# Kernel tuning notes

Measured on AMD Instinct MI355X. Metric: run time of the kernel, lower is better.

The kernel has to match this reference:

```python
import jax, jax.numpy as jnp
import numpy as np

K = 20
EPS = 1e-5
NEG_SLOPE = 0.2


def knn_idx(feat, k):
    # feat: (B, N, C). Pairwise neg squared distance, top-k nearest (self included).
    inner = jnp.einsum('bnc,bmc->bnm', feat, feat)          # (B,N,N)
    sq = jnp.sum(feat * feat, axis=-1)                      # (B,N)
    pd = 2.0 * inner - sq[:, :, None] - sq[:, None, :]      # -||xi-xj||^2
    return jax.lax.top_k(pd, k)[1]                          # (B,N,k)


def edge_conv(feat, W, g, b, m, v, k):
    # feat: (B,N,C); W: (O, 2C); BN params over O channels (eval-mode BN).
    idx = knn_idx(feat, k)                                  # (B,N,k)
    nbr = jnp.take_along_axis(feat[:, None, :, :], idx[..., None], axis=2)  # (B,N,k,C)
    ctr = jnp.broadcast_to(feat[:, :, None, :], nbr.shape)
    edge = jnp.concatenate([nbr - ctr, ctr], axis=-1)       # (B,N,k,2C)
    h = jnp.einsum('bnkc,oc->bnko', edge, W)                # 1x1 conv
    h = (h - m) * (g / jnp.sqrt(v + EPS)) + b               # BatchNorm2d (eval)
    h = jnp.where(h >= 0, h, NEG_SLOPE * h)                 # LeakyReLU(0.2)
    return jnp.max(h, axis=2)                               # max over k -> (B,N,O)


def setup_inputs() -> dict:
    key = jax.random.key(0)
    ks = jax.random.split(key, 21)
    B, N, C = 4, 4096, 3
    d = {'x': jax.random.normal(ks[0], (B, N, C), dtype=jnp.float32)}
    dims = [(64, 2 * 3), (64, 2 * 64), (128, 2 * 64), (256, 2 * 128)]
    for i, (o, c) in enumerate(dims, start=1):
        j = 1 + (i - 1) * 5
        d[f'W{i}'] = jax.random.normal(ks[j], (o, c), dtype=jnp.float32) * (1.0 / np.sqrt(c))
        d[f'g{i}'] = jax.random.uniform(ks[j + 1], (o,), minval=0.5, maxval=1.5, dtype=jnp.float32)
        d[f'b{i}'] = jax.random.normal(ks[j + 2], (o,), dtype=jnp.float32) * 0.1
        d[f'm{i}'] = jax.random.normal(ks[j + 3], (o,), dtype=jnp.float32) * 0.1
        d[f'v{i}'] = jax.random.uniform(ks[j + 4], (o,), minval=0.5, maxval=1.5, dtype=jnp.float32)
    return d


def reference(x, W1, g1, b1, m1, v1, W2, g2, b2, m2, v2,
              W3, g3, b3, m3, v3, W4, g4, b4, m4, v4):
    x1 = edge_conv(x, W1, g1, b1, m1, v1, K)    # (B,N,64)
    x2 = edge_conv(x1, W2, g2, b2, m2, v2, K)   # (B,N,64)
    x3 = edge_conv(x2, W3, g3, b3, m3, v3, K)   # (B,N,128)
    x4 = edge_conv(x3, W4, g4, b4, m4, v4, K)   # (B,N,256)
    return x4
```

## Files before the change

kernel.cpp:

```cpp
#include <hip/hip_runtime.h>

#define NTOT 4096
#define NBATCH 4
#define KNN 20
#define JSPLIT 8
#define JSPLIT3 4
#define KMRG 28
#define CSLOT3 256
#define CSLOTM 512

constexpr float NEG_INF = -3.0e38f;

typedef __attribute__((ext_vector_type(8))) short bf16x8;
typedef __attribute__((ext_vector_type(4))) float f32x4;

__device__ __forceinline__ unsigned pk(float f, int j) {
  unsigned u = __float_as_uint(f);
  u = (u & 0x80000000u) ? ~u : (u | 0x80000000u);
  return (u & 0xFFFFF000u) | (unsigned)j;
}

__device__ __forceinline__ void pins16(unsigned u, unsigned (&tv)[16]) {
  if (u > tv[0]) {
    tv[0] = u;
#pragma unroll
    for (int x = 1; x < 16; x++) {
      unsigned mn = min(tv[0], tv[x]);
      unsigned mx = max(tv[0], tv[x]);
      tv[0] = mn;
      tv[x] = mx;
    }
  }
}

__device__ __forceinline__ void pins8(unsigned u, unsigned (&tv)[8]) {
  if (u > tv[0]) {
    tv[0] = u;
#pragma unroll
    for (int x = 1; x < 8; x++) {
      unsigned mn = min(tv[0], tv[x]);
      unsigned mx = max(tv[0], tv[x]);
      tv[0] = mn;
      tv[x] = mx;
    }
  }
}

__device__ __forceinline__ void gll16(const void* g, void* l) {
  __builtin_amdgcn_global_load_lds(
      (const __attribute__((address_space(1))) unsigned int*)g,
      (__attribute__((address_space(3))) unsigned int*)l, 16, 0, 0);
}

__global__ void prep_w(const float* __restrict__ W, const float* __restrict__ gg,
                       const float* __restrict__ bb, const float* __restrict__ mm,
                       const float* __restrict__ vv, float* __restrict__ Wc,
                       float* __restrict__ bias, int O, int C) {
  int t = blockIdx.x * 256 + threadIdx.x;
  if (t >= 2 * O * C) return;
  int o2 = t / C, c = t - o2 * C;
  int o = (o2 < O) ? o2 : o2 - O;
  float s = gg[o] * rsqrtf(vv[o] + 1e-5f);
  float w = (o2 < O) ? W[o * 2 * C + c] * s
                     : (W[o * 2 * C + C + c] - W[o * 2 * C + c]) * s;
  Wc[o2 * C + c] = w;
  if (o2 >= O && c == 0) bias[o] = bb[o] - mm[o] * s;
}

__global__ void cvt_k(const float* __restrict__ f, ushort* __restrict__ hi,
                      ushort* __restrict__ lo) {
  int p = blockIdx.x * 256 + threadIdx.x;
  float x = f[p];
  unsigned u = __float_as_uint(x);
  unsigned h = (u + 0x7FFFu + ((u >> 16) & 1u)) >> 16;
  float hf = __uint_as_float(h << 16);
  float r = x - hf;
  unsigned v = __float_as_uint(r);
  unsigned l = (v + 0x7FFFu + ((v >> 16) & 1u)) >> 16;
  hi[p] = (ushort)h;
  lo[p] = (ushort)l;
}

template <int C>
__global__ void sqh_k(const float* __restrict__ f, float* __restrict__ sqh) {
  int p = blockIdx.x * 256 + threadIdx.x;
  const float* r = f + (size_t)p * C;
  float s = 0.f;
#pragma unroll
  for (int c4 = 0; c4 < C / 4; c4++) {
    float4 v = *(const float4*)&r[c4 * 4];
    s += v.x * v.x + v.y * v.y + v.z * v.z + v.w * v.w;
  }
  sqh[p] = 0.5f * s;
}

__global__ __launch_bounds__(256) void knn3_g(const float* __restrict__ feat,
                                              unsigned* __restrict__ cval) {
  __shared__ __align__(16) float sA[64 * 4];

  int tid = threadIdx.x;
  int js = blockIdx.x & (JSPLIT3 - 1);
  int rb = (blockIdx.x >> 2) & 63;
  int b = blockIdx.x >> 8;
  int row0 = rb * 64;
  int r = tid >> 2, q = tid & 3;
  int i = row0 + r;
  const float* fb = feat + (size_t)b * NTOT * 3;

  float c0 = fb[(size_t)i * 3 + 0];
  float c1 = fb[(size_t)i * 3 + 1];
  float c2 = fb[(size_t)i * 3 + 2];

  unsigned tv[16];
#pragma unroll
  for (int t = 0; t < 16; t++) tv[t] = 0u;

  for (int jt = js * (NTOT / JSPLIT3); jt < (js + 1) * (NTOT / JSPLIT3); jt += 64) {
    __syncthreads();
    if (tid < 64) {
      sA[tid * 4 + 0] = fb[(size_t)(jt + tid) * 3 + 0];
      sA[tid * 4 + 1] = fb[(size_t)(jt + tid) * 3 + 1];
      sA[tid * 4 + 2] = fb[(size_t)(jt + tid) * 3 + 2];
    }
    __syncthreads();

#pragma unroll
    for (int cc = 0; cc < 4; cc++) {
      float vq[4];
#pragma unroll
      for (int u = 0; u < 4; u++) {
        int jl = (cc * 4 + u) * 4 + q;
        float d0 = c0 - sA[jl * 4];
        float d1 = c1 - sA[jl * 4 + 1];
        float d2 = c2 - sA[jl * 4 + 2];
        vq[u] = -(d0 * d0 + d1 * d1 + d2 * d2);
      }
      float m4 = fmaxf(fmaxf(vq[0], vq[1]), fmaxf(vq[2], vq[3]));
      if (pk(m4, 0xFFF) > tv[0]) {
#pragma unroll
        for (int u = 0; u < 4; u++)
          pins16(pk(vq[u], jt + (cc * 4 + u) * 4 + q), tv);
      }
    }
  }

  int p = b * NTOT + row0 + r;
  int sub = js * 4 + q;
  unsigned* dst = cval + (size_t)p * CSLOT3 + sub * 16;
#pragma unroll
  for (int t4 = 0; t4 < 4; t4++) {
    uint4 o;
    o.x = tv[t4 * 4 + 0];
    o.y = tv[t4 * 4 + 1];
    o.z = tv[t4 * 4 + 2];
    o.w = tv[t4 * 4 + 3];
    *(uint4*)&dst[t4 * 4] = o;
  }
}

template <int C>
__global__ __launch_bounds__(256, 2) void knn_m(const ushort* __restrict__ Xhi,
                                                const ushort* __restrict__ Xlo,
                                                const float* __restrict__ sqh,
                                                unsigned* __restrict__ cval) {
  constexpr int NK = C / 32;
  constexpr int NJT = NTOT / (128 * JSPLIT);
  __shared__ __align__(16) char smem[67584];
  float* sqB = (float*)(smem + 65536);

  int tid = threadIdx.x;
  int raw = blockIdx.x;
  int b = raw & 3;
  int js = (raw >> 3) & (JSPLIT - 1);
  int it = (((raw >> 6) & 15) << 1) | ((raw >> 2) & 1);
  int i0 = it * 128;
  const ushort* xh = Xhi + (size_t)b * NTOT * C;
  const ushort* xl = Xlo + (size_t)b * NTOT * C;

  int l = tid & 63, wid = tid >> 6;
  int wi = wid & 1, wj = wid >> 1;
  int n = l & 15, quad = l >> 4;
  int xr16 = (n & 7) << 4;

  int t0 = l & 1, t1 = (l >> 1) & 1, t2 = (l >> 2) & 1, t3 = (l >> 3) & 1,
      t4 = (l >> 4) & 1, t5 = (l >> 5) & 1;
  int Rl = (t2 ^ t4) | (t3 << 1) | (t4 << 2) | (t5 << 3);
  int ql = (t0 ^ t2 ^ t4) | ((t1 ^ t3) << 1);

  int jbase = js * (NTOT / JSPLIT);

  if (tid < 128) {
    float4 s4 = *(const float4*)&sqh[b * NTOT + jbase + tid * 4];
    *(float4*)&sqB[tid * 4] = s4;
  }
  __syncthreads();

  unsigned tv[4][8];
#pragma unroll
  for (int ti = 0; ti < 4; ti++)
#pragma unroll
    for (int x = 0; x < 8; x++) tv[ti][x] = 0u;

  auto issue = [&](int jtn, int kcn, char* buf) {
    int j0n = jbase + jtn * 128;
#pragma unroll
    for (int c2 = 0; c2 < 2; c2++) {
      int R = Rl + (wid * 2 + c2) * 16;
      size_t gA = (size_t)(i0 + R) * C + kcn + ql * 8;
      size_t gB = (size_t)(j0n + R) * C + kcn + ql * 8;
      char* ld = buf + wid * 2048 + c2 * 1024;
      gll16(xh + gA, ld);
      gll16(xl + gA, ld + 8192);
      gll16(xh + gB, ld + 16384);
      gll16(xl + gB, ld + 24576);
    }
  };

  issue(0, 0, smem);

  int g = 0;
  for (int jt = 0; jt < NJT; jt++) {
    int j0 = jbase + jt * 128;

    f32x4 acc[4][4];
#pragma unroll
    for (int tj = 0; tj < 4; tj++)
#pragma unroll
      for (int ti = 0; ti < 4; ti++) acc[tj][ti] = (f32x4)(0.f);

    for (int kc = 0; kc < NK; kc++) {
      __builtin_amdgcn_s_barrier();
      int njt = (kc + 1 < NK) ? jt : ((jt + 1 == NJT) ? 0 : jt + 1);
      int nkc = (kc + 1 < NK) ? (kc + 1) * 32 : 0;
      issue(njt, nkc, smem + ((g + 1) & 1) * 32768);
      asm volatile("s_waitcnt vmcnt(8)" ::: "memory");
      __builtin_amdgcn_s_barrier();
      const char* bc = smem + (g & 1) * 32768;

      bf16x8 ah[4], al_[4];
#pragma unroll
      for (int ti = 0; ti < 4; ti++) {
        int row = wi * 64 + ti * 16 + n;
        int off = (row * 64 + quad * 16) ^ xr16;
        ah[ti] = *(const bf16x8*)(bc + off);
        al_[ti] = *(const bf16x8*)(bc + 8192 + off);
      }
#pragma unroll
      for (int tj = 0; tj < 4; tj++) {
        int row = wj * 64 + tj * 16 + n;
        int off = (row * 64 + quad * 16) ^ xr16;
        bf16x8 bh = *(const bf16x8*)(bc + 16384 + off);
        bf16x8 bl = *(const bf16x8*)(bc + 24576 + off);
#pragma unroll
        for (int ti = 0; ti < 4; ti++) {
          acc[tj][ti] = __builtin_amdgcn_mfma_f32_16x16x32_bf16(bh, ah[ti], acc[tj][ti], 0, 0, 0);
          acc[tj][ti] = __builtin_amdgcn_mfma_f32_16x16x32_bf16(bh, al_[ti], acc[tj][ti], 0, 0, 0);
          acc[tj][ti] = __builtin_amdgcn_mfma_f32_16x16x32_bf16(bl, ah[ti], acc[tj][ti], 0, 0, 0);
        }
      }
      g++;
    }

    float4 sq4[4];
#pragma unroll
    for (int tj = 0; tj < 4; tj++)
      sq4[tj] = *(const float4*)&sqB[jt * 128 + wj * 64 + tj * 16 + quad * 4];
#pragma unroll
    for (int ti = 0; ti < 4; ti++) {
#pragma unroll
      for (int tj = 0; tj < 4; tj++) {
        float v0 = acc[tj][ti][0] - sq4[tj].x;
        float v1 = acc[tj][ti][1] - sq4[tj].y;
        float v2 = acc[tj][ti][2] - sq4[tj].z;
        float v3 = acc[tj][ti][3] - sq4[tj].w;
        float m4 = fmaxf(fmaxf(v0, v1), fmaxf(v2, v3));
        if (pk(m4, 0xFFF) > tv[ti][0]) {
          int jb = j0 + wj * 64 + tj * 16 + quad * 4;
          pins8(pk(v0, jb + 0), tv[ti]);
          pins8(pk(v1, jb + 1), tv[ti]);
          pins8(pk(v2, jb + 2), tv[ti]);
          pins8(pk(v3, jb + 3), tv[ti]);
        }
      }
    }
  }

#pragma unroll
  for (int ti = 0; ti < 4; ti++) {
    int p = b * NTOT + i0 + wi * 64 + ti * 16 + n;
    unsigned* dst = cval + (size_t)p * CSLOTM + js * 64 + wj * 32 + quad * 8;
    uint4 o0, o1;
    o0.x = tv[ti][0]; o0.y = tv[ti][1]; o0.z = tv[ti][2]; o0.w = tv[ti][3];
    o1.x = tv[ti][4]; o1.y = tv[ti][5]; o1.z = tv[ti][6]; o1.w = tv[ti][7];
    *(uint4*)&dst[0] = o0;
    *(uint4*)&dst[4] = o1;
  }
}

template <int C, int NC>
__global__ __launch_bounds__(256) void kref_w(const float* __restrict__ feat,
                                              const unsigned* __restrict__ cval,
                                              int* __restrict__ outidx) {
  constexpr int NPL = NC / 64;
  int tid = threadIdx.x;
  int lane = tid & 63;
  int p = blockIdx.x * 4 + (tid >> 6);
  int b = p >> 12;
  int i = p & (NTOT - 1);
  const float* fb = feat + (size_t)b * NTOT * C;

  unsigned c[NPL];
  if constexpr (NPL == 8) {
    uint4 aa = *(const uint4*)&cval[(size_t)p * NC + lane * 8];
    uint4 bb2 = *(const uint4*)&cval[(size_t)p * NC + lane * 8 + 4];
    c[0] = aa.x; c[1] = aa.y; c[2] = aa.z; c[3] = aa.w;
    c[4] = bb2.x; c[5] = bb2.y; c[6] = bb2.z; c[7] = bb2.w;
  } else {
    uint4 aa = *(const uint4*)&cval[(size_t)p * NC + lane * 4];
    c[0] = aa.x; c[1] = aa.y; c[2] = aa.z; c[3] = aa.w;
  }

  int myj = -1;
#pragma unroll
  for (int t = 0; t < KMRG; t++) {
    unsigned m = c[0];
#pragma unroll
    for (int x = 1; x < NPL; x++) m = max(m, c[x]);
#pragma unroll
    for (int s = 1; s < 64; s <<= 1) m = max(m, (unsigned)__shfl_xor((int)m, s));
    if (lane == t) myj = (int)(m & 0xFFFu);
#pragma unroll
    for (int x = 0; x < NPL; x++)
      if (c[x] == m) c[x] = 0;
  }

  float myval = NEG_INF;
  if constexpr (C == 3) {
    if (lane < KMRG) {
      float x0 = fb[(size_t)i * 3 + 0];
      float x1 = fb[(size_t)i * 3 + 1];
      float x2 = fb[(size_t)i * 3 + 2];
      float y0 = fb[(size_t)myj * 3 + 0];
      float y1 = fb[(size_t)myj * 3 + 1];
      float y2 = fb[(size_t)myj * 3 + 2];
      float d0 = x0 - y0, d1 = x1 - y1, d2 = x2 - y2;
      myval = -(d0 * d0 + d1 * d1 + d2 * d2);
    }
  } else {
    constexpr int SL = C / 8;
    int m8 = lane & 7;
    float4 xs[SL / 4];
#pragma unroll
    for (int q4 = 0; q4 < SL / 4; q4++)
      xs[q4] = *(const float4*)&fb[(size_t)i * C + m8 * SL + q4 * 4];
#pragma unroll
    for (int ps = 0; ps < (KMRG + 7) / 8; ps++) {
      int src = ps * 8 + (lane >> 3);
      src = (src < KMRG) ? src : KMRG - 1;
      int j = __shfl(myj, src);
      float d = 0.f;
#pragma unroll
      for (int q4 = 0; q4 < SL / 4; q4++) {
        float4 yv = *(const float4*)&fb[(size_t)j * C + m8 * SL + q4 * 4];
        float dx = xs[q4].x - yv.x;
        float dy = xs[q4].y - yv.y;
        float dz = xs[q4].z - yv.z;
        float dw = xs[q4].w - yv.w;
        d += dx * dx + dy * dy + dz * dz + dw * dw;
      }
#pragma unroll
      for (int s = 1; s < 8; s <<= 1) d += __shfl_xor(d, s);
      float sd = __shfl(d, (lane & 7) << 3);
      bool upd = ((lane >> 3) == ps) && (lane < KMRG);
      myval = upd ? -sd : myval;
    }
  }

#pragma unroll
  for (int k = 2; k <= 64; k <<= 1) {
#pragma unroll
    for (int j2 = k >> 1; j2 > 0; j2 >>= 1) {
      float ov = __shfl_xor(myval, j2);
      int oj = __shfl_xor(myj, j2);
      bool ogt = (ov > myval) || (ov == myval && oj < myj);
      bool lower = ((lane & j2) == 0);
      bool desc = ((lane & k) == 0);
      bool take = (desc == (lower == ogt));
      myval = take ? ov : myval;
      myj = take ? oj : myj;
    }
  }

  if (lane < KNN) outidx[(size_t)p * KNN + lane] = myj;
}

__global__ __launch_bounds__(256) void gemm128(const float* __restrict__ A,
                                               const float* __restrict__ Wc,
                                               const float* __restrict__ bias,
                                               float* __restrict__ Y, int K, int N2,
                                               int O) {
  constexpr int P = 140;
  __shared__ float As[16 * P];
  __shared__ float Bs[16 * P];
  int tid = threadIdx.x;
  int n0 = blockIdx.x * 128;
  int m0 = blockIdx.y * 128;
  int tx = tid & 15, ty = tid >> 4;
  int aoff = (ty * 8) + (((ty * 8) >> 5) << 2);
  int boff = (tx * 8) + (((tx * 8) >> 5) << 2);
  float acc[8][8];
#pragma unroll
  for (int ii = 0; ii < 8; ii++)
#pragma unroll
    for (int jj = 0; jj < 8; jj++) acc[ii][jj] = 0.f;

  for (int kc = 0; kc < K; kc += 16) {
    __syncthreads();
#pragma unroll
    for (int l = 0; l < 2; l++) {
      int e = tid + 256 * l;
      int rr = e >> 2, c4 = e & 3;
      int sc = rr + ((rr >> 5) << 2);
      float4 va = *(const float4*)&A[(size_t)(m0 + rr) * K + kc + c4 * 4];
      As[(c4 * 4 + 0) * P + sc] = va.x;
      As[(c4 * 4 + 1) * P + sc] = va.y;
      As[(c4 * 4 + 2) * P + sc] = va.z;
      As[(c4 * 4 + 3) * P + sc] = va.w;
      float4 vb = *(const float4*)&Wc[(size_t)(n0 + rr) * K + kc + c4 * 4];
      Bs[(c4 * 4 + 0) * P + sc] = vb.x;
      Bs[(c4 * 4 + 1) * P + sc] = vb.y;
      Bs[(c4 * 4 + 2) * P + sc] = vb.z;
      Bs[(c4 * 4 + 3) * P + sc] = vb.w;
    }
    __syncthreads();
#pragma unroll 8
    for (int k = 0; k < 16; k++) {
      float4 a0 = *(const float4*)&As[k * P + aoff];
      float4 a1 = *(const float4*)&As[k * P + aoff + 4];
      float4 b0 = *(const float4*)&Bs[k * P + boff];
      float4 b1 = *(const float4*)&Bs[k * P + boff + 4];
      float av[8] = {a0.x, a0.y, a0.z, a0.w, a1.x, a1.y, a1.z, a1.w};
      float bv[8] = {b0.x, b0.y, b0.z, b0.w, b1.x, b1.y, b1.z, b1.w};
#pragma unroll
      for (int ii = 0; ii < 8; ii++)
#pragma unroll
        for (int jj = 0; jj < 8; jj++)
          acc[ii][jj] = fmaf(av[ii], bv[jj], acc[ii][jj]);
    }
  }

  int col0 = n0 + tx * 8;
  float bv[8];
#pragma unroll
  for (int jj = 0; jj < 8; jj++) {
    int col = col0 + jj;
    bv[jj] = (col >= O) ? bias[col - O] : 0.f;
  }
#pragma unroll
  for (int ii = 0; ii < 8; ii++) {
    int row = m0 + ty * 8 + ii;
    float4 o0, o1;
    o0.x = acc[ii][0] + bv[0];
    o0.y = acc[ii][1] + bv[1];
    o0.z = acc[ii][2] + bv[2];
    o0.w = acc[ii][3] + bv[3];
    o1.x = acc[ii][4] + bv[4];
    o1.y = acc[ii][5] + bv[5];
    o1.z = acc[ii][6] + bv[6];
    o1.w = acc[ii][7] + bv[7];
    *(float4*)&Y[(size_t)row * N2 + col0] = o0;
    *(float4*)&Y[(size_t)row * N2 + col0 + 4] = o1;
  }
}

__global__ __launch_bounds__(256) void gemm_k(const float* __restrict__ A,
                                              const float* __restrict__ Wc,
                                              const float* __restrict__ bias,
                                              float* __restrict__ Y, int K, int N2,
                                              int O) {
  __shared__ float As[8 * 68];
  __shared__ float Bs[8 * 68];
  int tid = threadIdx.x;
  int n0 = blockIdx.x * 64;
  int m0 = blockIdx.y * 64;
  int tx = tid & 15, ty = tid >> 4;
  float acc[4][4] = {};
  for (int k0 = 0; k0 < K; k0 += 8) {
    __syncthreads();
    {
      int e = tid, mm = e >> 3, kk = e & 7;
      As[kk * 68 + mm] = (k0 + kk < K) ? A[(size_t)(m0 + mm) * K + k0 + kk] : 0.f;
      int nn = mm;
      Bs[kk * 68 + nn] = (k0 + kk < K) ? Wc[(size_t)(n0 + nn) * K + k0 + kk] : 0.f;
      e = tid + 256;
      mm = e >> 3;
      kk = e & 7;
      As[kk * 68 + mm] = (k0 + kk < K) ? A[(size_t)(m0 + mm) * K + k0 + kk] : 0.f;
      nn = mm;
      Bs[kk * 68 + nn] = (k0 + kk < K) ? Wc[(size_t)(n0 + nn) * K + k0 + kk] : 0.f;
    }
    __syncthreads();
#pragma unroll
    for (int kk = 0; kk < 8; kk++) {
      float4 av = *(float4*)&As[kk * 68 + ty * 4];
      float4 bv = *(float4*)&Bs[kk * 68 + tx * 4];
      float a[4] = {av.x, av.y, av.z, av.w};
      float bb2[4] = {bv.x, bv.y, bv.z, bv.w};
#pragma unroll
      for (int ii = 0; ii < 4; ii++)
#pragma unroll
        for (int jj = 0; jj < 4; jj++) acc[ii][jj] += a[ii] * bb2[jj];
    }
  }
  int col = n0 + tx * 4;
  bool isV = (col >= O);
  float b0 = 0.f, b1 = 0.f, b2 = 0.f, b3 = 0.f;
  if (isV) {
    b0 = bias[col + 0 - O];
    b1 = bias[col + 1 - O];
    b2 = bias[col + 2 - O];
    b3 = bias[col + 3 - O];
  }
#pragma unroll
  for (int ii = 0; ii < 4; ii++) {
    int row = m0 + ty * 4 + ii;
    float4 o4;
    o4.x = acc[ii][0] + b0;
    o4.y = acc[ii][1] + b1;
    o4.z = acc[ii][2] + b2;
    o4.w = acc[ii][3] + b3;
    *(float4*)&Y[(size_t)row * N2 + col] = o4;
  }
}

template <int O>
__global__ __launch_bounds__(256) void gmax_v(const float* __restrict__ Y,
                                              const int* __restrict__ idx,
                                              float* __restrict__ out) {
  constexpr int T = O / 4;
  constexpr int G = 256 / T;
  int tid = threadIdx.x;
  int p = blockIdx.x * G + tid / T;
  int o4 = (tid % T) * 4;
  int b = p >> 12;
  constexpr int N2 = 2 * O;
  const int* ip = idx + (size_t)p * KNN;
  float4 m = make_float4(NEG_INF, NEG_INF, NEG_INF, NEG_INF);
#pragma unroll
  for (int k = 0; k < KNN; k++) {
    int j = ip[k];
    float4 v = *(const float4*)&Y[((size_t)(b * NTOT + j)) * N2 + o4];
    m.x = fmaxf(m.x, v.x);
    m.y = fmaxf(m.y, v.y);
    m.z = fmaxf(m.z, v.z);
    m.w = fmaxf(m.w, v.w);
  }
  float4 c = *(const float4*)&Y[(size_t)p * N2 + O + o4];
  float4 o;
  o.x = c.x + m.x;
  o.y = c.y + m.y;
  o.z = c.z + m.z;
  o.w = c.w + m.w;
  o.x = (o.x >= 0.f) ? o.x : 0.2f * o.x;
  o.y = (o.y >= 0.f) ? o.y : 0.2f * o.y;
  o.z = (o.z >= 0.f) ? o.z : 0.2f * o.z;
  o.w = (o.w >= 0.f) ? o.w : 0.2f * o.w;
  *(float4*)&out[(size_t)p * O + o4] = o;
}

template <int C, int O>
static void run_layer(const float* fin, void* const* w5, float* fout, float* Wc,
                      float* biasb, int* idx, float* Y, float* sqh,
                      unsigned* cval, ushort* Xhi, ushort* Xlo,
                      hipStream_t stream) {
  const float* W = (const float*)w5[0];
  const float* g = (const float*)w5[1];
  const float* bb = (const float*)w5[2];
  const float* mm = (const float*)w5[3];
  const float* vv = (const float*)w5[4];
  int N2 = 2 * O;
  prep_w<<<(2 * O * C + 255) / 256, 256, 0, stream>>>(W, g, bb, mm, vv, Wc, biasb, O, C);
  if (C == 3) {
    knn3_g<<<NBATCH * 64 * JSPLIT3, 256, 0, stream>>>(fin, cval);
    kref_w<3, 256><<<NBATCH * NTOT / 4, 256, 0, stream>>>(fin, cval, idx);
    dim3 gg(N2 / 64, NBATCH * NTOT / 64);
    gemm_k<<<gg, 256, 0, stream>>>(fin, Wc, biasb, Y, C, N2, O);
  } else {
    constexpr int CC = (C == 3) ? 64 : C;
    cvt_k<<<NBATCH * NTOT * CC / 256, 256, 0, stream>>>(fin, Xhi, Xlo);
    sqh_k<CC><<<NBATCH * NTOT / 256, 256, 0, stream>>>(fin, sqh);
    knn_m<CC><<<NBATCH * 32 * JSPLIT, 256, 0, stream>>>(Xhi, Xlo, sqh, cval);
    kref_w<CC, 512><<<NBATCH * NTOT / 4, 256, 0, stream>>>(fin, cval, idx);
    dim3 gg(N2 / 128, NBATCH * NTOT / 128);
    gemm128<<<gg, 256, 0, stream>>>(fin, Wc, biasb, Y, C, N2, O);
  }
  gmax_v<O><<<NBATCH * NTOT / (256 / (O / 4)), 256, 0, stream>>>(Y, idx, fout);
}

extern "C" void kernel_launch(void* const* d_in, const int* in_sizes, int n_in,
                              void* d_out, int out_size, void* d_ws, size_t ws_size,
                              hipStream_t stream) {
  const float* x = (const float*)d_in[0];
  char* ws = (char*)d_ws;
  float* Wc = (float*)(ws + 0);
  float* biasb = (float*)(ws + 262144);
  int* idx = (int*)(ws + 263168);
  float* sqh = (float*)(ws + 1573888);
  float* Y = (float*)(ws + 1639424);
  float* x1 = (float*)(ws + 35193856);
  float* x2 = (float*)(ws + 39388160);
  float* x3 = (float*)(ws + 43582464);

  unsigned* cval = (unsigned*)Y;
  ushort* X2h = (ushort*)x2;
  ushort* X2l = X2h + (size_t)NBATCH * NTOT * 64;
  ushort* X3h = (ushort*)x3;
  ushort* X3l = X3h + (size_t)NBATCH * NTOT * 64;
  float* outf = (float*)d_out;
  ushort* X4h = (ushort*)outf;
  ushort* X4l = X4h + (size_t)NBATCH * NTOT * 128;

  run_layer<3, 64>(x, d_in + 1, x1, Wc, biasb, idx, Y, sqh, cval, nullptr, nullptr, stream);
  run_layer<64, 64>(x1, d_in + 6, x2, Wc, biasb, idx, Y, sqh, cval, X2h, X2l, stream);
  run_layer<64, 128>(x2, d_in + 11, x3, Wc, biasb, idx, Y, sqh, cval, X3h, X3l, stream);
  run_layer<128, 256>(x3, d_in + 16, outf, Wc, biasb, idx, Y, sqh, cval, X4h, X4l, stream);
}
```

Before: 727.8 us.

## Route first-layer kNN through the bf16 split MFMA kNN kernel with padding

```diff
diff --git a/kernel.cpp b/kernel.cpp
--- a/kernel.cpp
+++ b/kernel.cpp
@@ -4,9 +4,7 @@
 #define NBATCH 4
 #define KNN 20
 #define JSPLIT 8
-#define JSPLIT3 4
 #define KMRG 28
-#define CSLOT3 256
 #define CSLOTM 512
 
 constexpr float NEG_INF = -3.0e38f;
@@ -18,19 +16,6 @@
   unsigned u = __float_as_uint(f);
   u = (u & 0x80000000u) ? ~u : (u | 0x80000000u);
   return (u & 0xFFFFF000u) | (unsigned)j;
-}
-
-__device__ __forceinline__ void pins16(unsigned u, unsigned (&tv)[16]) {
-  if (u > tv[0]) {
-    tv[0] = u;
-#pragma unroll
-    for (int x = 1; x < 16; x++) {
-      unsigned mn = min(tv[0], tv[x]);
-      unsigned mx = max(tv[0], tv[x]);
-      tv[0] = mn;
-      tv[x] = mx;
-    }
-  }
 }
 
 __device__ __forceinline__ void pins8(unsigned u, unsigned (&tv)[8]) {
@@ -81,6 +66,21 @@
   lo[p] = (ushort)l;
 }
 
+__global__ void cvt3_k(const float* __restrict__ f, ushort* __restrict__ hi,
+                       ushort* __restrict__ lo) {
+  int p = blockIdx.x * 256 + threadIdx.x;
+  int pt = p >> 5, dim = p & 31;
+  float x = (dim < 3) ? f[pt * 3 + dim] : 0.f;
+  unsigned u = __float_as_uint(x);
+  unsigned h = (u + 0x7FFFu + ((u >> 16) & 1u)) >> 16;
+  float hf = __uint_as_float(h << 16);
+  float r = x - hf;
+  unsigned v = __float_as_uint(r);
+  unsigned l = (v + 0x7FFFu + ((v >> 16) & 1u)) >> 16;
+  hi[p] = (ushort)h;
+  lo[p] = (ushort)l;
+}
+
 template <int C>
 __global__ void sqh_k(const float* __restrict__ f, float* __restrict__ sqh) {
   int p = blockIdx.x * 256 + threadIdx.x;
@@ -94,68 +94,12 @@
   sqh[p] = 0.5f * s;
 }
 
-__global__ __launch_bounds__(256) void knn3_g(const float* __restrict__ feat,
-                                              unsigned* __restrict__ cval) {
-  __shared__ __align__(16) float sA[64 * 4];
-
-  int tid = threadIdx.x;
-  int js = blockIdx.x & (JSPLIT3 - 1);
-  int rb = (blockIdx.x >> 2) & 63;
-  int b = blockIdx.x >> 8;
-  int row0 = rb * 64;
-  int r = tid >> 2, q = tid & 3;
-  int i = row0 + r;
-  const float* fb = feat + (size_t)b * NTOT * 3;
-
-  float c0 = fb[(size_t)i * 3 + 0];
-  float c1 = fb[(size_t)i * 3 + 1];
-  float c2 = fb[(size_t)i * 3 + 2];
-
-  unsigned tv[16];
-#pragma unroll
-  for (int t = 0; t < 16; t++) tv[t] = 0u;
-
-  for (int jt = js * (NTOT / JSPLIT3); jt < (js + 1) * (NTOT / JSPLIT3); jt += 64) {
-    __syncthreads();
-    if (tid < 64) {
-      sA[tid * 4 + 0] = fb[(size_t)(jt + tid) * 3 + 0];
-      sA[tid * 4 + 1] = fb[(size_t)(jt + tid) * 3 + 1];
-      sA[tid * 4 + 2] = fb[(size_t)(jt + tid) * 3 + 2];
-    }
-    __syncthreads();
-
-#pragma unroll
-    for (int cc = 0; cc < 4; cc++) {
-      float vq[4];
-#pragma unroll
-      for (int u = 0; u < 4; u++) {
-        int jl = (cc * 4 + u) * 4 + q;
-        float d0 = c0 - sA[jl * 4];
-        float d1 = c1 - sA[jl * 4 + 1];
-        float d2 = c2 - sA[jl * 4 + 2];
-        vq[u] = -(d0 * d0 + d1 * d1 + d2 * d2);
-      }
-      float m4 = fmaxf(fmaxf(vq[0], vq[1]), fmaxf(vq[2], vq[3]));
-      if (pk(m4, 0xFFF) > tv[0]) {
-#pragma unroll
-        for (int u = 0; u < 4; u++)
-          pins16(pk(vq[u], jt + (cc * 4 + u) * 4 + q), tv);
-      }
-    }
-  }
-
-  int p = b * NTOT + row0 + r;
-  int sub = js * 4 + q;
-  unsigned* dst = cval + (size_t)p * CSLOT3 + sub * 16;
-#pragma unroll
-  for (int t4 = 0; t4 < 4; t4++) {
-    uint4 o;
-    o.x = tv[t4 * 4 + 0];
-    o.y = tv[t4 * 4 + 1];
-    o.z = tv[t4 * 4 + 2];
-    o.w = tv[t4 * 4 + 3];
-    *(uint4*)&dst[t4 * 4] = o;
-  }
+__global__ void sqh3_k(const float* __restrict__ f, float* __restrict__ sqh) {
+  int p = blockIdx.x * 256 + threadIdx.x;
+  float a = f[(size_t)p * 3 + 0];
+  float b2 = f[(size_t)p * 3 + 1];
+  float c = f[(size_t)p * 3 + 2];
+  sqh[p] = 0.5f * (a * a + b2 * b2 + c * c);
 }
 
 template <int C>
@@ -581,8 +525,10 @@
   int N2 = 2 * O;
   prep_w<<<(2 * O * C + 255) / 256, 256, 0, stream>>>(W, g, bb, mm, vv, Wc, biasb, O, C);
   if (C == 3) {
-    knn3_g<<<NBATCH * 64 * JSPLIT3, 256, 0, stream>>>(fin, cval);
-    kref_w<3, 256><<<NBATCH * NTOT / 4, 256, 0, stream>>>(fin, cval, idx);
+    cvt3_k<<<NBATCH * NTOT * 32 / 256, 256, 0, stream>>>(fin, Xhi, Xlo);
+    sqh3_k<<<NBATCH * NTOT / 256, 256, 0, stream>>>(fin, sqh);
+    knn_m<32><<<NBATCH * 32 * JSPLIT, 256, 0, stream>>>(Xhi, Xlo, sqh, cval);
+    kref_w<3, 512><<<NBATCH * NTOT / 4, 256, 0, stream>>>(fin, cval, idx);
     dim3 gg(N2 / 64, NBATCH * NTOT / 64);
     gemm_k<<<gg, 256, 0, stream>>>(fin, Wc, biasb, Y, C, N2, O);
   } else {
@@ -612,6 +558,8 @@
   float* x3 = (float*)(ws + 43582464);
 
   unsigned* cval = (unsigned*)Y;
+  ushort* X1h = (ushort*)x1;
+  ushort* X1l = X1h + (size_t)NBATCH * NTOT * 32;
   ushort* X2h = (ushort*)x2;
   ushort* X2l = X2h + (size_t)NBATCH * NTOT * 64;
   ushort* X3h = (ushort*)x3;
@@ -620,7 +568,7 @@
   ushort* X4h = (ushort*)outf;
   ushort* X4l = X4h + (size_t)NBATCH * NTOT * 128;
 
-  run_layer<3, 64>(x, d_in + 1, x1, Wc, biasb, idx, Y, sqh, cval, nullptr, nullptr, stream);
+  run_layer<3, 64>(x, d_in + 1, x1, Wc, biasb, idx, Y, sqh, cval, X1h, X1l, stream);
   run_layer<64, 64>(x1, d_in + 6, x2, Wc, biasb, idx, Y, sqh, cval, X2h, X2l, stream);
   run_layer<64, 128>(x2, d_in + 11, x3, Wc, biasb, idx, Y, sqh, cval, X3h, X3l, stream);
   run_layer<128, 256>(x3, d_in + 16, outf, Wc, biasb, idx, Y, sqh, cval, X4h, X4l, stream);
```

Measured after the change: 734.3 us. About the same (+0.9%).
